# Kernel tuning notes

Hardware: AMD Instinct MI355X
Metric: run time of the kernel (lower is better)

## Reference

```python
import jax, jax.numpy as jnp
import numpy as np

N_NODES = 100000
N_EDGES = 1000000
D = 64
N_LAYERS = 3
LN_EPS = 1e-5


def setup_inputs() -> dict:
    key = jax.random.key(0)
    ks = jax.random.split(key, 12)
    s = 1.0 / np.sqrt(D)
    return {
        "feats": jax.random.normal(ks[0], (N_NODES, D), jnp.float32),
        "src": jax.random.randint(ks[1], (N_EDGES,), 0, N_NODES, jnp.int32),
        "dst": jax.random.randint(ks[2], (N_EDGES,), 0, N_NODES, jnp.int32),
        # GraphConv weights/biases (stacked over layers; in==hid==out==D)
        "conv_W": jax.random.normal(ks[3], (N_LAYERS, D, D), jnp.float32) * s,
        "conv_b": jnp.zeros((N_LAYERS, D), jnp.float32),
        # residual Linear per layer
        "res_W": jax.random.normal(ks[4], (N_LAYERS, D, D), jnp.float32) * s,
        "res_b": jnp.zeros((N_LAYERS, D), jnp.float32),
        # LayerNorm affine per layer
        "ln_g": jnp.ones((N_LAYERS, D), jnp.float32),
        "ln_b": jnp.zeros((N_LAYERS, D), jnp.float32),
        # final linear_prediction
        "pred_W": jax.random.normal(ks[5], (D, D), jnp.float32) * s,
        "pred_b": jnp.zeros((D,), jnp.float32),
    }


def _layer_norm(h, g, b):
    mu = jnp.mean(h, axis=-1, keepdims=True)
    var = jnp.mean(jnp.square(h - mu), axis=-1, keepdims=True)
    return (h - mu) * jax.lax.rsqrt(var + LN_EPS) * g + b


def reference(feats, src, dst, conv_W, conv_b, res_W, res_b, ln_g, ln_b, pred_W, pred_b):
    n = feats.shape[0]
    ones = jnp.ones(src.shape[0], feats.dtype)
    # DGL GraphConv norm='both', degrees clamped to >= 1
    out_deg = jnp.clip(jax.ops.segment_sum(ones, src, num_segments=n), 1.0, None)
    in_deg = jnp.clip(jax.ops.segment_sum(ones, dst, num_segments=n), 1.0, None)
    out_norm = jax.lax.rsqrt(out_deg)[:, None]  # [N,1]
    in_norm = jax.lax.rsqrt(in_deg)[:, None]

    h = feats
    h_final = jnp.zeros_like(feats)
    for i in range(N_LAYERS):
        # GraphConv: scale src, sum-aggregate over edges, scale dst, linear
        msg = (h * out_norm)[src]                                   # [E, D]
        agg = jax.ops.segment_sum(msg, dst, num_segments=n) * in_norm
        conv = agg @ conv_W[i] + conv_b[i]
        # residual linear + LayerNorm + relu (dropout p=0) + JK accumulate
        h = conv + h @ res_W[i] + res_b[i]
        h = jax.nn.relu(_layer_norm(h, ln_g[i], ln_b[i]))
        h_final = h_final + h
    return h_final @ pred_W + pred_b
```

## Files before the change

kernel.cpp:

```cpp
#include <hip/hip_runtime.h>
#include <hip/hip_bf16.h>

#define DD 64
#define NBLK 128
#define MAXBUK 1024
#define BSHIFT 7
#define NB3 64

typedef __attribute__((ext_vector_type(8))) short short8v;
typedef __attribute__((ext_vector_type(4))) float f32x4;

__device__ __forceinline__ unsigned pk_bf16(float a, float b) {
    __hip_bfloat162 h = __float22bfloat162_rn(make_float2(a, b));
    unsigned u; __builtin_memcpy(&u, &h, 4); return u;
}
__device__ __forceinline__ short f2bf_s(float f) {
    union { float f; unsigned u; } x; x.f = f;
    unsigned r = x.u + 0x7fff + ((x.u >> 16) & 1);
    return (short)(r >> 16);
}
__device__ __forceinline__ float bf_lo(unsigned u) { return __int_as_float(u << 16); }
__device__ __forceinline__ float bf_hi(unsigned u) { return __int_as_float(u & 0xffff0000u); }
__device__ __forceinline__ short8v u4_to_s8(uint4 u) {
    union { uint4 u; short8v s; } x; x.u = u; return x.s;
}


__global__ __launch_bounds__(256) void part_count(
        const int* __restrict__ src, const int* __restrict__ dst,
        int* __restrict__ cnt, int E, int nbuk, int ce) {
    __shared__ int hd[MAXBUK], hs[MAXBUK];
    for (int i = threadIdx.x; i < MAXBUK; i += 256) { hd[i] = 0; hs[i] = 0; }
    __syncthreads();
    int e0 = blockIdx.x * ce;
    int e1 = min(e0 + ce, E);
    for (int e = e0 + (int)threadIdx.x; e < e1; e += 256) {
        atomicAdd(&hd[dst[e] >> BSHIFT], 1);
        atomicAdd(&hs[src[e] >> BSHIFT], 1);
    }
    __syncthreads();
    int L2 = nbuk * NBLK;
    for (int b = threadIdx.x; b < nbuk; b += 256) {
        cnt[b * NBLK + blockIdx.x]      = hd[b];
        cnt[L2 + b * NBLK + blockIdx.x] = hs[b];
    }
}

__global__ void scan1p(int* __restrict__ a, int* __restrict__ bsums, int L) {
    __shared__ int tmp[256];
    int gid = blockIdx.x * 256 + threadIdx.x;
    int v = (gid < L) ? a[gid] : 0;
    tmp[threadIdx.x] = v;
    __syncthreads();
    for (int off = 1; off < 256; off <<= 1) {
        int t = (threadIdx.x >= off) ? tmp[threadIdx.x - off] : 0;
        __syncthreads();
        tmp[threadIdx.x] += t;
        __syncthreads();
    }
    if (gid < L) a[gid] = tmp[threadIdx.x] - v;
    if (threadIdx.x == 255) bsums[blockIdx.x] = tmp[255];
}
__global__ void scan2p(int* __restrict__ bsums, int nb) {
    __shared__ int tmp[1024];
    int v = (threadIdx.x < (unsigned)nb) ? bsums[threadIdx.x] : 0;
    tmp[threadIdx.x] = v;
    __syncthreads();
    for (int off = 1; off < 1024; off <<= 1) {
        int t = (threadIdx.x >= off) ? tmp[threadIdx.x - off] : 0;
        __syncthreads();
        tmp[threadIdx.x] += t;
        __syncthreads();
    }
    if (threadIdx.x < (unsigned)nb) bsums[threadIdx.x] = tmp[threadIdx.x] - v;
}
__global__ void scan3p(int* __restrict__ a, const int* __restrict__ bsums, int L) {
    int gid = blockIdx.x * 256 + threadIdx.x;
    if (gid < L) a[gid] += bsums[blockIdx.x];
}

__global__ __launch_bounds__(256) void part_scatter(
        const int* __restrict__ src, const int* __restrict__ dst,
        const int* __restrict__ ofs,
        unsigned int* __restrict__ partD, unsigned char* __restrict__ partS,
        int E, int nbuk, int ce) {
    __shared__ int cd[MAXBUK], cs[MAXBUK];
    int L2 = nbuk * NBLK;
    for (int b = threadIdx.x; b < nbuk; b += 256) {
        cd[b] = ofs[b * NBLK + blockIdx.x];
        cs[b] = ofs[L2 + b * NBLK + blockIdx.x] - E;
    }
    __syncthreads();
    int e0 = blockIdx.x * ce;
    int e1 = min(e0 + ce, E);
    for (int e = e0 + (int)threadIdx.x; e < e1; e += 256) {
        int s = src[e], d = dst[e];
        int pd = atomicAdd(&cd[d >> BSHIFT], 1);
        partD[pd] = ((unsigned)(d & 127) << 17) | (unsigned)s;
        int ps = atomicAdd(&cs[s >> BSHIFT], 1);
        partS[ps] = (unsigned char)(s & 127);
    }
}

__global__ __launch_bounds__(256) void bucket_hist(
        const unsigned int* __restrict__ partD, const int* __restrict__ ofs,
        int* __restrict__ deg, int E, int nbuk, int n) {
    __shared__ int h[128];
    int b = blockIdx.x, tid = threadIdx.x;
    int e0 = ofs[b * NBLK];
    int e1 = (b + 1 < nbuk) ? ofs[(b + 1) * NBLK] : E;
    if (tid < 128) h[tid] = 0;
    __syncthreads();
    for (int e = e0 + tid; e < e1; e += 256)
        atomicAdd(&h[partD[e] >> 17], 1);
    __syncthreads();
    if (tid < 128) {
        int v = (b << BSHIFT) + tid;
        if (v < n) deg[v] = h[tid];
    }
}

__global__ __launch_bounds__(256) void bucket_deg(
        const unsigned char* __restrict__ partS, const int* __restrict__ ofs,
        int* __restrict__ outdeg, int E, int nbuk, int n) {
    __shared__ int h[128];
    int b = blockIdx.x, tid = threadIdx.x;
    int L2 = nbuk * NBLK;
    int f0 = ofs[L2 + b * NBLK] - E;
    int f1 = (b + 1 < nbuk) ? ofs[L2 + (b + 1) * NBLK] - E : E;
    if (tid < 128) h[tid] = 0;
    __syncthreads();
    for (int e = f0 + tid; e < f1; e += 256)
        atomicAdd(&h[(int)partS[e]], 1);
    __syncthreads();
    if (tid < 128) {
        int v = (b << BSHIFT) + tid;
        if (v < n) outdeg[v] = h[tid];
    }
}

__global__ __launch_bounds__(256) void dhist(const int* __restrict__ deg,
                                             int* __restrict__ cnt2, int N, int chunk) {
    __shared__ int h2[256];
    h2[threadIdx.x] = 0;
    __syncthreads();
    int b = blockIdx.x;
    int v0 = b * chunk, v1 = min(v0 + chunk, N);
    for (int v = v0 + (int)threadIdx.x; v < v1; v += 256)
        atomicAdd(&h2[min(deg[v], 255)], 1);
    __syncthreads();
    cnt2[threadIdx.x * NB3 + b] = h2[threadIdx.x];
}
__global__ __launch_bounds__(256) void dscatter(const int* __restrict__ deg,
                                                const int* __restrict__ cnt2,
                                                int* __restrict__ perm, int N, int chunk) {
    __shared__ int cu2[256];
    int b = blockIdx.x;
    cu2[threadIdx.x] = cnt2[threadIdx.x * NB3 + b];
    __syncthreads();
    int v0 = b * chunk, v1 = min(v0 + chunk, N);
    for (int v = v0 + (int)threadIdx.x; v < v1; v += 256) {
        int pos = atomicAdd(&cu2[min(deg[v], 255)], 1);
        perm[pos] = v;
    }
}
__global__ void invperm(const int* __restrict__ perm, int* __restrict__ inv, int N) {
    int i = blockIdx.x * 256 + threadIdx.x;
    if (i < N) inv[perm[i]] = i;
}
__global__ void sortgath(const int* __restrict__ perm, const int* __restrict__ deg,
                         const int* __restrict__ outdeg,
                         int* __restrict__ rowptr2, float* __restrict__ inn2,
                         float* __restrict__ rs2, float* __restrict__ outn2,
                         int N, int E) {
    int i = blockIdx.x * 256 + threadIdx.x;
    if (i < N) {
        int p = perm[i];
        int d = deg[p];
        int od = outdeg[p];
        rowptr2[i] = d;
        inn2[i] = rsqrtf((float)max(d, 1));
        float odc = (float)max(od, 1);
        outn2[i] = rsqrtf(odc);
        rs2[i]   = sqrtf(odc);
        if (i == 0) rowptr2[N] = E;
    }
}

__global__ __launch_bounds__(256) void bucket_scatter(
        const unsigned int* __restrict__ partD, const int* __restrict__ ofs,
        const int* __restrict__ rowptr2, const int* __restrict__ inv,
        int* __restrict__ esrc2, int E, int nbuk, int n) {
    __shared__ int cu[128];
    int b = blockIdx.x, tid = threadIdx.x;
    int e0 = ofs[b * NBLK];
    int e1 = (b + 1 < nbuk) ? ofs[(b + 1) * NBLK] : E;
    if (tid < 128) {
        int v = (b << BSHIFT) + tid;
        cu[tid] = (v < n) ? rowptr2[inv[v]] : 0;
    }
    __syncthreads();
    for (int e = e0 + tid; e < e1; e += 256) {
        unsigned u = partD[e];
        int p = atomicAdd(&cu[u >> 17], 1);
        esrc2[p] = inv[u & 0x1FFFFu];
    }
}

__global__ void scale_perm(const float* __restrict__ feats, const float* __restrict__ outn2,
                           const int* __restrict__ perm,
                           unsigned short* __restrict__ hs, int n) {
    int idx = blockIdx.x * blockDim.x + threadIdx.x;
    if (idx < n * 8) {
        int v = idx >> 3, c = idx & 7;
        int p = perm[v];
        float s = outn2[v];
        const float4* fp = (const float4*)(feats + (size_t)p * DD) + c * 2;
        float4 f0 = fp[0], f1 = fp[1];
        uint4 o;
        o.x = pk_bf16(f0.x * s, f0.y * s); o.y = pk_bf16(f0.z * s, f0.w * s);
        o.z = pk_bf16(f1.x * s, f1.y * s); o.w = pk_bf16(f1.z * s, f1.w * s);
        ((uint4*)hs)[idx] = o;
    }
}

__global__ __launch_bounds__(256) void gcn_kernel(
    const int* __restrict__ rowptr, const int* __restrict__ esrc,
    const int* __restrict__ perm,
    const float* __restrict__ inn, const float* __restrict__ rs,
    const float* __restrict__ outn,
    const unsigned short* __restrict__ hs_in,
    const float* __restrict__ Wc, const float* __restrict__ bc,
    const float* __restrict__ Wr, const float* __restrict__ br,
    const float* __restrict__ Wp, const float* __restrict__ pb,
    const float* __restrict__ g, const float* __restrict__ bb,
    unsigned short* __restrict__ hs_out, float* __restrict__ h_final,
    float* __restrict__ pred_out,
    int first, int last, int n)
{
    __shared__ __align__(16) short sWf[24 * 64 * 8];
    __shared__ __align__(16) short sXa[4][16 * 72];
    __shared__ float sEps[4 * 64];

    int lane = threadIdx.x & 63;
    int wave = threadIdx.x >> 6;
    int q   = lane & 15;
    int gg  = lane >> 4;
    int q8  = lane & 7;
    int o8  = lane >> 3;

    for (int idx = threadIdx.x; idx < 64; idx += blockDim.x) {
        sEps[idx]       = bc[idx] + br[idx];
        sEps[64 + idx]  = g[idx];
        sEps[128 + idx] = bb[idx];
        sEps[192 + idx] = pb[idx];
    }
    for (int f = wave * 6; f < wave * 6 + 6; ++f) {
        int mat = f >> 3, ft = (f >> 1) & 3, kc = f & 1;
        const float* Ws = (mat == 0) ? Wc : (mat == 1) ? Wr : Wp;
        int feat = ft * 16 + q;
        int k0 = kc * 32 + gg * 8;
        short8v fr;
        #pragma unroll
        for (int j = 0; j < 8; ++j) fr[j] = f2bf_s(Ws[(k0 + j) * DD + feat]);
        *(short8v*)&sWf[(f * 64 + lane) * 8] = fr;
    }
    __syncthreads();

    short* xrow_w = &sXa[wave][0];
    const short8v* wf = (const short8v*)sWf;
    int wgid = blockIdx.x * 4 + wave;
    int nwav = gridDim.x * 4;
    int ngrp = (n + 15) >> 4;

    for (int grp = wgid; grp < ngrp; grp += nwav) {
        int vbase = grp << 4;
        int vo = vbase + q;
        int vsel = min(vo, n - 1);

        const uint4* hrow = (const uint4*)(hs_in + (size_t)vsel * DD);
        uint4 bh0u = hrow[gg];
        uint4 bh1u = hrow[4 + gg];
        float rsv  = rs[vsel];
        float innv = inn[vsel];

        int rp = rowptr[min(vbase + min(lane, 16), n)];
        int stA = __shfl(rp, o8);     int dgA = __shfl(rp, o8 + 1) - stA;
        int stB = __shfl(rp, o8 + 8); int dgB = __shfl(rp, o8 + 9) - stB;

        #pragma unroll
        for (int hh = 0; hh < 2; ++hh) {
            int st = hh ? stB : stA;
            int dg = hh ? dgB : dgA;
            int mdg = dg;
            mdg = max(mdg, __shfl_xor(mdg, 8));
            mdg = max(mdg, __shfl_xor(mdg, 16));
            mdg = max(mdg, __shfl_xor(mdg, 32));

            float a[8];
            #pragma unroll
            for (int c = 0; c < 8; ++c) a[c] = 0.0f;

            int id0 = (0 < dg) ? esrc[st + 0] : 0;  float m0 = (0 < dg) ? 1.f : 0.f;
            int id1 = (1 < dg) ? esrc[st + 1] : 0;  float m1 = (1 < dg) ? 1.f : 0.f;
            int id2 = (2 < dg) ? esrc[st + 2] : 0;  float m2 = (2 < dg) ? 1.f : 0.f;
            int id3 = (3 < dg) ? esrc[st + 3] : 0;  float m3 = (3 < dg) ? 1.f : 0.f;

            for (int t = 0; t < mdg; t += 4) {
                uint4 r0 = *(const uint4*)(hs_in + (size_t)id0 * DD + q8 * 8);
                uint4 r1 = *(const uint4*)(hs_in + (size_t)id1 * DD + q8 * 8);
                uint4 r2 = *(const uint4*)(hs_in + (size_t)id2 * DD + q8 * 8);
                uint4 r3 = *(const uint4*)(hs_in + (size_t)id3 * DD + q8 * 8);
                float c0 = m0, c1 = m1, c2 = m2, c3 = m3;
                int t4 = t + 4;
                id0 = (t4 + 0 < dg) ? esrc[st + t4 + 0] : 0;  m0 = (t4 + 0 < dg) ? 1.f : 0.f;
                id1 = (t4 + 1 < dg) ? esrc[st + t4 + 1] : 0;  m1 = (t4 + 1 < dg) ? 1.f : 0.f;
                id2 = (t4 + 2 < dg) ? esrc[st + t4 + 2] : 0;  m2 = (t4 + 2 < dg) ? 1.f : 0.f;
                id3 = (t4 + 3 < dg) ? esrc[st + t4 + 3] : 0;  m3 = (t4 + 3 < dg) ? 1.f : 0.f;
                a[0] = fmaf(bf_lo(r0.x), c0, a[0]); a[1] = fmaf(bf_hi(r0.x), c0, a[1]);
                a[2] = fmaf(bf_lo(r0.y), c0, a[2]); a[3] = fmaf(bf_hi(r0.y), c0, a[3]);
                a[4] = fmaf(bf_lo(r0.z), c0, a[4]); a[5] = fmaf(bf_hi(r0.z), c0, a[5]);
                a[6] = fmaf(bf_lo(r0.w), c0, a[6]); a[7] = fmaf(bf_hi(r0.w), c0, a[7]);
                a[0] = fmaf(bf_lo(r1.x), c1, a[0]); a[1] = fmaf(bf_hi(r1.x), c1, a[1]);
                a[2] = fmaf(bf_lo(r1.y), c1, a[2]); a[3] = fmaf(bf_hi(r1.y), c1, a[3]);
                a[4] = fmaf(bf_lo(r1.z), c1, a[4]); a[5] = fmaf(bf_hi(r1.z), c1, a[5]);
                a[6] = fmaf(bf_lo(r1.w), c1, a[6]); a[7] = fmaf(bf_hi(r1.w), c1, a[7]);
                a[0] = fmaf(bf_lo(r2.x), c2, a[0]); a[1] = fmaf(bf_hi(r2.x), c2, a[1]);
                a[2] = fmaf(bf_lo(r2.y), c2, a[2]); a[3] = fmaf(bf_hi(r2.y), c2, a[3]);
                a[4] = fmaf(bf_lo(r2.z), c2, a[4]); a[5] = fmaf(bf_hi(r2.z), c2, a[5]);
                a[6] = fmaf(bf_lo(r2.w), c2, a[6]); a[7] = fmaf(bf_hi(r2.w), c2, a[7]);
                a[0] = fmaf(bf_lo(r3.x), c3, a[0]); a[1] = fmaf(bf_hi(r3.x), c3, a[1]);
                a[2] = fmaf(bf_lo(r3.y), c3, a[2]); a[3] = fmaf(bf_hi(r3.y), c3, a[3]);
                a[4] = fmaf(bf_lo(r3.z), c3, a[4]); a[5] = fmaf(bf_hi(r3.z), c3, a[5]);
                a[6] = fmaf(bf_lo(r3.w), c3, a[6]); a[7] = fmaf(bf_hi(r3.w), c3, a[7]);
            }

            uint4 w4;
            w4.x = pk_bf16(a[0], a[1]); w4.y = pk_bf16(a[2], a[3]);
            w4.z = pk_bf16(a[4], a[5]); w4.w = pk_bf16(a[6], a[7]);
            *(uint4*)&xrow_w[(hh * 8 + o8) * 72 + q8 * 8] = w4;
        }

        const short* xr = &xrow_w[q * 72];
        short8v ba0 = *(const short8v*)&xr[gg * 8];
        short8v ba1 = *(const short8v*)&xr[32 + gg * 8];
        short8v sh0 = u4_to_s8(bh0u);
        short8v sh1 = u4_to_s8(bh1u);

        f32x4 accC[4], accR[4];
        #pragma unroll
        for (int ft = 0; ft < 4; ++ft) {
            f32x4 c = {0.f, 0.f, 0.f, 0.f};
            c = __builtin_amdgcn_mfma_f32_16x16x32_bf16(wf[(ft * 2 + 0) * 64 + lane], ba0, c, 0, 0, 0);
            c = __builtin_amdgcn_mfma_f32_16x16x32_bf16(wf[(ft * 2 + 1) * 64 + lane], ba1, c, 0, 0, 0);
            accC[ft] = c;
            f32x4 r = {0.f, 0.f, 0.f, 0.f};
            r = __builtin_amdgcn_mfma_f32_16x16x32_bf16(wf[(8 + ft * 2 + 0) * 64 + lane], sh0, r, 0, 0, 0);
            r = __builtin_amdgcn_mfma_f32_16x16x32_bf16(wf[(8 + ft * 2 + 1) * 64 + lane], sh1, r, 0, 0, 0);
            accR[ft] = r;
        }

        f32x4 ac[4];
        #pragma unroll
        for (int ft = 0; ft < 4; ++ft) {
            float4 b4 = *(const float4*)&sEps[ft * 16 + gg * 4];
            ac[ft][0] = fmaf(innv, accC[ft][0], fmaf(rsv, accR[ft][0], b4.x));
            ac[ft][1] = fmaf(innv, accC[ft][1], fmaf(rsv, accR[ft][1], b4.y));
            ac[ft][2] = fmaf(innv, accC[ft][2], fmaf(rsv, accR[ft][2], b4.z));
            ac[ft][3] = fmaf(innv, accC[ft][3], fmaf(rsv, accR[ft][3], b4.w));
        }
        float s = 0.f;
        #pragma unroll
        for (int ft = 0; ft < 4; ++ft) s += ac[ft][0] + ac[ft][1] + ac[ft][2] + ac[ft][3];
        s += __shfl_xor(s, 16); s += __shfl_xor(s, 32);
        float mu = s * (1.0f / 64.0f);
        float vsum = 0.f;
        #pragma unroll
        for (int ft = 0; ft < 4; ++ft) {
            #pragma unroll
            for (int r = 0; r < 4; ++r) { float d = ac[ft][r] - mu; vsum += d * d; }
        }
        vsum += __shfl_xor(vsum, 16); vsum += __shfl_xor(vsum, 32);
        float rinv = rsqrtf(vsum * (1.0f / 64.0f) + 1e-5f);

        float4 yv[4];
        #pragma unroll
        for (int ft = 0; ft < 4; ++ft) {
            float4 g4 = *(const float4*)&sEps[64 + ft * 16 + gg * 4];
            float4 c4 = *(const float4*)&sEps[128 + ft * 16 + gg * 4];
            yv[ft].x = fmaxf((ac[ft][0] - mu) * rinv * g4.x + c4.x, 0.f);
            yv[ft].y = fmaxf((ac[ft][1] - mu) * rinv * g4.y + c4.y, 0.f);
            yv[ft].z = fmaxf((ac[ft][2] - mu) * rinv * g4.z + c4.z, 0.f);
            yv[ft].w = fmaxf((ac[ft][3] - mu) * rinv * g4.w + c4.w, 0.f);
        }

        if (!last) {
            if (vo < n) {
                float on = outn[vo];
                #pragma unroll
                for (int ft = 0; ft < 4; ++ft) {
                    size_t off = (size_t)vo * DD + ft * 16 + gg * 4;
                    uint2 p;
                    p.x = pk_bf16(yv[ft].x * on, yv[ft].y * on);
                    p.y = pk_bf16(yv[ft].z * on, yv[ft].w * on);
                    *(uint2*)&hs_out[off] = p;
                    if (first) {
                        *(float4*)&h_final[off] = yv[ft];
                    } else {
                        float4 hf = *(const float4*)&h_final[off];
                        hf.x += yv[ft].x; hf.y += yv[ft].y;
                        hf.z += yv[ft].z; hf.w += yv[ft].w;
                        *(float4*)&h_final[off] = hf;
                    }
                }
            }
        } else {
            int pvo = perm[vsel];
            #pragma unroll
            for (int ft = 0; ft < 4; ++ft) {
                float4 hf = make_float4(0.f, 0.f, 0.f, 0.f);
                if (vo < n) {
                    float4 old = *(const float4*)&h_final[(size_t)vo * DD + ft * 16 + gg * 4];
                    hf.x = old.x + yv[ft].x; hf.y = old.y + yv[ft].y;
                    hf.z = old.z + yv[ft].z; hf.w = old.w + yv[ft].w;
                }
                uint2 p;
                p.x = pk_bf16(hf.x, hf.y);
                p.y = pk_bf16(hf.z, hf.w);
                *(uint2*)&xrow_w[q * 72 + ft * 16 + gg * 4] = p;
            }
            short8v bp0 = *(const short8v*)&xr[gg * 8];
            short8v bp1 = *(const short8v*)&xr[32 + gg * 8];
            #pragma unroll
            for (int ft = 0; ft < 4; ++ft) {
                f32x4 p = {0.f, 0.f, 0.f, 0.f};
                p = __builtin_amdgcn_mfma_f32_16x16x32_bf16(wf[(16 + ft * 2 + 0) * 64 + lane], bp0, p, 0, 0, 0);
                p = __builtin_amdgcn_mfma_f32_16x16x32_bf16(wf[(16 + ft * 2 + 1) * 64 + lane], bp1, p, 0, 0, 0);
                if (vo < n) {
                    float4 b4 = *(const float4*)&sEps[192 + ft * 16 + gg * 4];
                    float4 o = make_float4(p[0] + b4.x, p[1] + b4.y, p[2] + b4.z, p[3] + b4.w);
                    *(float4*)&pred_out[(size_t)pvo * DD + ft * 16 + gg * 4] = o;
                }
            }
        }
    }
}

extern "C" void kernel_launch(void* const* d_in, const int* in_sizes, int n_in,
                              void* d_out, int out_size, void* d_ws, size_t ws_size,
                              hipStream_t stream) {
    const float* feats  = (const float*)d_in[0];
    const int*   src    = (const int*)d_in[1];
    const int*   dst    = (const int*)d_in[2];
    const float* conv_W = (const float*)d_in[3];
    const float* conv_b = (const float*)d_in[4];
    const float* res_W  = (const float*)d_in[5];
    const float* res_b  = (const float*)d_in[6];
    const float* ln_g   = (const float*)d_in[7];
    const float* ln_b   = (const float*)d_in[8];
    const float* pred_W = (const float*)d_in[9];
    const float* pred_b = (const float*)d_in[10];

    int N = in_sizes[0] / DD;
    int E = in_sizes[1];

    int nbuk = (N + (1 << BSHIFT) - 1) >> BSHIFT;
    int ce   = (E + NBLK - 1) / NBLK;
    int L    = nbuk * NBLK * 2;
    int nb   = (L + 255) / 256;
    int chunk3 = (N + NB3 - 1) / NB3;
    int L3   = 256 * NB3;
    int nb3  = (L3 + 255) / 256;
    int nbN  = (N + 255) / 256;

    int*   rowptr2 = (int*)d_ws;
    int*   cnt    = rowptr2 + (N + 1);
    int*   bsums  = cnt + MAXBUK * NBLK * 2;
    int*   esrc2  = bsums + 1024;
    float* outn2  = (float*)(esrc2 + E);
    float* inn2   = outn2 + N;
    float* rs2    = inn2 + N;
    int*   deg    = (int*)(rs2 + N);
    int*   outdeg = deg + N;
    int*   perm   = outdeg + N;
    int*   inv    = perm + N;
    int*   cnt2   = inv + N;
    float* base   = (float*)(((uintptr_t)(cnt2 + 16384) + 15) & ~(uintptr_t)15);
    unsigned short* hsA = (unsigned short*)base;
    unsigned short* hsB = (unsigned short*)(base + (size_t)N * 32);
    float* hfin  = base + (size_t)N * 64;
    unsigned int*  partD = (unsigned int*)hfin;
    unsigned char* partS = (unsigned char*)(partD + E);

    part_count   <<<NBLK, 256, 0, stream>>>(src, dst, cnt, E, nbuk, ce);
    scan1p       <<<nb, 256, 0, stream>>>(cnt, bsums, L);
    scan2p       <<<1, 1024, 0, stream>>>(bsums, nb);
    scan3p       <<<nb, 256, 0, stream>>>(cnt, bsums, L);
    part_scatter <<<NBLK, 256, 0, stream>>>(src, dst, cnt, partD, partS, E, nbuk, ce);
    bucket_hist  <<<nbuk, 256, 0, stream>>>(partD, cnt, deg, E, nbuk, N);
    bucket_deg   <<<nbuk, 256, 0, stream>>>(partS, cnt, outdeg, E, nbuk, N);
    dhist        <<<NB3, 256, 0, stream>>>(deg, cnt2, N, chunk3);
    scan1p       <<<nb3, 256, 0, stream>>>(cnt2, bsums, L3);
    scan2p       <<<1, 1024, 0, stream>>>(bsums, nb3);
    scan3p       <<<nb3, 256, 0, stream>>>(cnt2, bsums, L3);
    dscatter     <<<NB3, 256, 0, stream>>>(deg, cnt2, perm, N, chunk3);
    invperm      <<<nbN, 256, 0, stream>>>(perm, inv, N);
    sortgath     <<<nbN, 256, 0, stream>>>(perm, deg, outdeg, rowptr2, inn2, rs2, outn2, N, E);
    scan1p       <<<nbN, 256, 0, stream>>>(rowptr2, bsums, N);
    scan2p       <<<1, 1024, 0, stream>>>(bsums, nbN);
    scan3p       <<<nbN, 256, 0, stream>>>(rowptr2, bsums, N);
    bucket_scatter<<<nbuk, 256, 0, stream>>>(partD, cnt, rowptr2, inv, esrc2, E, nbuk, N);
    scale_perm   <<<(N * 8 + 255) / 256, 256, 0, stream>>>(feats, outn2, perm, hsA, N);

    const unsigned short* ins[3]  = {hsA, hsB, hsA};
    unsigned short*       outs[3] = {hsB, hsA, hsB};
    for (int l = 0; l < 3; ++l) {
        gcn_kernel<<<1024, 256, 0, stream>>>(
            rowptr2, esrc2, perm, inn2, rs2, outn2, ins[l],
            conv_W + (size_t)l * DD * DD, conv_b + (size_t)l * DD,
            res_W  + (size_t)l * DD * DD, res_b  + (size_t)l * DD,
            pred_W, pred_b,
            ln_g   + (size_t)l * DD,      ln_b   + (size_t)l * DD,
            outs[l], hfin, (float*)d_out,
            (l == 0) ? 1 : 0, (l == 2) ? 1 : 0, N);
    }
}
```

Baseline: 326.1 us.

## Fuse preprocessing kernels, fold scan carry into consumers, sort edges per row

Merges in/out-degree histograms with the degree-bucket histogram, and fuses the degree scatter with the inverse permutation and norm gathering. Two scan-add passes are dropped by having consumers add block sums on the fly. This cuts the number of preprocessing launches and intermediate passes. It also adds a per-row quadratic sort of source indices, meant to give the gather better locality, and reverses group iteration order in the GCN kernel, at the cost of an extra kernel and O(d^2) work on high-degree rows.

New measurement: 364.1 us. 1.12x slower.

```diff
diff --git a/kernel.cpp b/kernel.cpp
--- a/kernel.cpp
+++ b/kernel.cpp
@@ -5,7 +5,6 @@
 #define NBLK 128
 #define MAXBUK 1024
 #define BSHIFT 7
-#define NB3 64
 
 typedef __attribute__((ext_vector_type(8))) short short8v;
 typedef __attribute__((ext_vector_type(4))) float f32x4;
@@ -23,6 +22,10 @@
 __device__ __forceinline__ float bf_hi(unsigned u) { return __int_as_float(u & 0xffff0000u); }
 __device__ __forceinline__ short8v u4_to_s8(uint4 u) {
     union { uint4 u; short8v s; } x; x.u = u; return x.s;
+}
+__device__ __forceinline__ int ofs_at(const int* __restrict__ c,
+                                      const int* __restrict__ bs, int i) {
+    return c[i] + bs[i >> 8];
 }
 
 
@@ -81,14 +84,14 @@
 
 __global__ __launch_bounds__(256) void part_scatter(
         const int* __restrict__ src, const int* __restrict__ dst,
-        const int* __restrict__ ofs,
+        const int* __restrict__ cnt, const int* __restrict__ bsA,
         unsigned int* __restrict__ partD, unsigned char* __restrict__ partS,
         int E, int nbuk, int ce) {
     __shared__ int cd[MAXBUK], cs[MAXBUK];
     int L2 = nbuk * NBLK;
     for (int b = threadIdx.x; b < nbuk; b += 256) {
-        cd[b] = ofs[b * NBLK + blockIdx.x];
-        cs[b] = ofs[L2 + b * NBLK + blockIdx.x] - E;
+        cd[b] = ofs_at(cnt, bsA, b * NBLK + blockIdx.x);
+        cs[b] = ofs_at(cnt, bsA, L2 + b * NBLK + blockIdx.x) - E;
     }
     __syncthreads();
     int e0 = blockIdx.x * ce;
@@ -102,99 +105,75 @@
     }
 }
 
-__global__ __launch_bounds__(256) void bucket_hist(
-        const unsigned int* __restrict__ partD, const int* __restrict__ ofs,
-        int* __restrict__ deg, int E, int nbuk, int n) {
-    __shared__ int h[128];
+__global__ __launch_bounds__(256) void bucket_histdeg(
+        const unsigned int* __restrict__ partD, const unsigned char* __restrict__ partS,
+        const int* __restrict__ cnt, const int* __restrict__ bsA,
+        int* __restrict__ deg, int* __restrict__ outdeg, int* __restrict__ cnt2,
+        int E, int nbuk, int n) {
+    __shared__ int hi[128], ho[128], h2[256];
     int b = blockIdx.x, tid = threadIdx.x;
-    int e0 = ofs[b * NBLK];
-    int e1 = (b + 1 < nbuk) ? ofs[(b + 1) * NBLK] : E;
-    if (tid < 128) h[tid] = 0;
-    __syncthreads();
+    if (tid < 128) { hi[tid] = 0; ho[tid] = 0; }
+    h2[tid] = 0;
+    __syncthreads();
+    int e0 = ofs_at(cnt, bsA, b * NBLK);
+    int e1 = (b + 1 < nbuk) ? ofs_at(cnt, bsA, (b + 1) * NBLK) : E;
     for (int e = e0 + tid; e < e1; e += 256)
-        atomicAdd(&h[partD[e] >> 17], 1);
+        atomicAdd(&hi[partD[e] >> 17], 1);
+    int L2 = nbuk * NBLK;
+    int f0 = ofs_at(cnt, bsA, L2 + b * NBLK) - E;
+    int f1 = (b + 1 < nbuk) ? ofs_at(cnt, bsA, L2 + (b + 1) * NBLK) - E : E;
+    for (int e = f0 + tid; e < f1; e += 256)
+        atomicAdd(&ho[(int)partS[e]], 1);
     __syncthreads();
     if (tid < 128) {
         int v = (b << BSHIFT) + tid;
-        if (v < n) deg[v] = h[tid];
-    }
-}
-
-__global__ __launch_bounds__(256) void bucket_deg(
-        const unsigned char* __restrict__ partS, const int* __restrict__ ofs,
-        int* __restrict__ outdeg, int E, int nbuk, int n) {
-    __shared__ int h[128];
+        if (v < n) {
+            deg[v] = hi[tid];
+            outdeg[v] = ho[tid];
+            atomicAdd(&h2[min(hi[tid], 255)], 1);
+        }
+    }
+    __syncthreads();
+    cnt2[tid * nbuk + b] = h2[tid];
+}
+
+__global__ __launch_bounds__(256) void dscatter_fused(
+        const int* __restrict__ deg, const int* __restrict__ outdeg,
+        const int* __restrict__ cnt2, const int* __restrict__ bsB,
+        int* __restrict__ perm, int* __restrict__ inv,
+        int* __restrict__ rowptr2, float* __restrict__ inn2,
+        float* __restrict__ outn2, float* __restrict__ rs2,
+        int nbuk, int n, int E) {
+    __shared__ int cu2[256];
     int b = blockIdx.x, tid = threadIdx.x;
-    int L2 = nbuk * NBLK;
-    int f0 = ofs[L2 + b * NBLK] - E;
-    int f1 = (b + 1 < nbuk) ? ofs[L2 + (b + 1) * NBLK] - E : E;
-    if (tid < 128) h[tid] = 0;
-    __syncthreads();
-    for (int e = f0 + tid; e < f1; e += 256)
-        atomicAdd(&h[(int)partS[e]], 1);
+    cu2[tid] = ofs_at(cnt2, bsB, tid * nbuk + b);
     __syncthreads();
     if (tid < 128) {
         int v = (b << BSHIFT) + tid;
-        if (v < n) outdeg[v] = h[tid];
-    }
-}
-
-__global__ __launch_bounds__(256) void dhist(const int* __restrict__ deg,
-                                             int* __restrict__ cnt2, int N, int chunk) {
-    __shared__ int h2[256];
-    h2[threadIdx.x] = 0;
-    __syncthreads();
-    int b = blockIdx.x;
-    int v0 = b * chunk, v1 = min(v0 + chunk, N);
-    for (int v = v0 + (int)threadIdx.x; v < v1; v += 256)
-        atomicAdd(&h2[min(deg[v], 255)], 1);
-    __syncthreads();
-    cnt2[threadIdx.x * NB3 + b] = h2[threadIdx.x];
-}
-__global__ __launch_bounds__(256) void dscatter(const int* __restrict__ deg,
-                                                const int* __restrict__ cnt2,
-                                                int* __restrict__ perm, int N, int chunk) {
-    __shared__ int cu2[256];
-    int b = blockIdx.x;
-    cu2[threadIdx.x] = cnt2[threadIdx.x * NB3 + b];
-    __syncthreads();
-    int v0 = b * chunk, v1 = min(v0 + chunk, N);
-    for (int v = v0 + (int)threadIdx.x; v < v1; v += 256) {
-        int pos = atomicAdd(&cu2[min(deg[v], 255)], 1);
-        perm[pos] = v;
-    }
-}
-__global__ void invperm(const int* __restrict__ perm, int* __restrict__ inv, int N) {
-    int i = blockIdx.x * 256 + threadIdx.x;
-    if (i < N) inv[perm[i]] = i;
-}
-__global__ void sortgath(const int* __restrict__ perm, const int* __restrict__ deg,
-                         const int* __restrict__ outdeg,
-                         int* __restrict__ rowptr2, float* __restrict__ inn2,
-                         float* __restrict__ rs2, float* __restrict__ outn2,
-                         int N, int E) {
-    int i = blockIdx.x * 256 + threadIdx.x;
-    if (i < N) {
-        int p = perm[i];
-        int d = deg[p];
-        int od = outdeg[p];
-        rowptr2[i] = d;
-        inn2[i] = rsqrtf((float)max(d, 1));
-        float odc = (float)max(od, 1);
-        outn2[i] = rsqrtf(odc);
-        rs2[i]   = sqrtf(odc);
-        if (i == 0) rowptr2[N] = E;
-    }
+        if (v < n) {
+            int d = deg[v];
+            int pos = atomicAdd(&cu2[min(d, 255)], 1);
+            perm[pos] = v;
+            inv[v] = pos;
+            rowptr2[pos] = d;
+            inn2[pos] = rsqrtf((float)max(d, 1));
+            float oc = (float)max(outdeg[v], 1);
+            outn2[pos] = rsqrtf(oc);
+            rs2[pos]   = sqrtf(oc);
+        }
+    }
+    if (b == 0 && tid == 0) rowptr2[n] = E;
 }
 
 __global__ __launch_bounds__(256) void bucket_scatter(
-        const unsigned int* __restrict__ partD, const int* __restrict__ ofs,
+        const unsigned int* __restrict__ partD,
+        const int* __restrict__ cnt, const int* __restrict__ bsA,
         const int* __restrict__ rowptr2, const int* __restrict__ inv,
-        int* __restrict__ esrc2, int E, int nbuk, int n) {
+        int* __restrict__ esrcT, int E, int nbuk, int n) {
     __shared__ int cu[128];
     int b = blockIdx.x, tid = threadIdx.x;
-    int e0 = ofs[b * NBLK];
-    int e1 = (b + 1 < nbuk) ? ofs[(b + 1) * NBLK] : E;
+    int e0 = ofs_at(cnt, bsA, b * NBLK);
+    int e1 = (b + 1 < nbuk) ? ofs_at(cnt, bsA, (b + 1) * NBLK) : E;
     if (tid < 128) {
         int v = (b << BSHIFT) + tid;
         cu[tid] = (v < n) ? rowptr2[inv[v]] : 0;
@@ -203,7 +182,24 @@
     for (int e = e0 + tid; e < e1; e += 256) {
         unsigned u = partD[e];
         int p = atomicAdd(&cu[u >> 17], 1);
-        esrc2[p] = inv[u & 0x1FFFFu];
+        esrcT[p] = inv[u & 0x1FFFFu];
+    }
+}
+
+__global__ void edge_sort(const int* __restrict__ rowptr2,
+                          const int* __restrict__ esrcT,
+                          int* __restrict__ esrc2, int n) {
+    int v = blockIdx.x * 256 + threadIdx.x;
+    if (v >= n) return;
+    int b0 = rowptr2[v], d = rowptr2[v + 1] - b0;
+    for (int i = 0; i < d; ++i) {
+        int ki = esrcT[b0 + i];
+        int pos = 0;
+        for (int j = 0; j < d; ++j) {
+            int kj = esrcT[b0 + j];
+            pos += (kj < ki) | ((kj == ki) & (j < i));
+        }
+        esrc2[b0 + pos] = ki;
     }
 }
 
@@ -273,7 +269,8 @@
     int nwav = gridDim.x * 4;
     int ngrp = (n + 15) >> 4;
 
-    for (int grp = wgid; grp < ngrp; grp += nwav) {
+    for (int g0 = wgid; g0 < ngrp; g0 += nwav) {
+        int grp = ngrp - 1 - g0;
         int vbase = grp << 4;
         int vo = vbase + q;
         int vsel = min(vo, n - 1);
@@ -468,49 +465,47 @@
     int ce   = (E + NBLK - 1) / NBLK;
     int L    = nbuk * NBLK * 2;
     int nb   = (L + 255) / 256;
-    int chunk3 = (N + NB3 - 1) / NB3;
-    int L3   = 256 * NB3;
+    int L3   = 256 * nbuk;
     int nb3  = (L3 + 255) / 256;
     int nbN  = (N + 255) / 256;
 
     int*   rowptr2 = (int*)d_ws;
     int*   cnt    = rowptr2 + (N + 1);
-    int*   bsums  = cnt + MAXBUK * NBLK * 2;
-    int*   esrc2  = bsums + 1024;
+    int*   bsA    = cnt + MAXBUK * NBLK * 2;
+    int*   bsB    = bsA + 1024;
+    int*   bsC    = bsB + 1024;
+    int*   esrc2  = bsC + 1024;
     float* outn2  = (float*)(esrc2 + E);
     float* inn2   = outn2 + N;
     float* rs2    = inn2 + N;
-    int*   deg    = (int*)(rs2 + N);
-    int*   outdeg = deg + N;
-    int*   perm   = outdeg + N;
-    int*   inv    = perm + N;
-    int*   cnt2   = inv + N;
-    float* base   = (float*)(((uintptr_t)(cnt2 + 16384) + 15) & ~(uintptr_t)15);
+    int*   perm   = (int*)(rs2 + N);
+    float* base   = (float*)(((uintptr_t)(perm + N) + 15) & ~(uintptr_t)15);
     unsigned short* hsA = (unsigned short*)base;
     unsigned short* hsB = (unsigned short*)(base + (size_t)N * 32);
     float* hfin  = base + (size_t)N * 64;
     unsigned int*  partD = (unsigned int*)hfin;
     unsigned char* partS = (unsigned char*)(partD + E);
-
-    part_count   <<<NBLK, 256, 0, stream>>>(src, dst, cnt, E, nbuk, ce);
-    scan1p       <<<nb, 256, 0, stream>>>(cnt, bsums, L);
-    scan2p       <<<1, 1024, 0, stream>>>(bsums, nb);
-    scan3p       <<<nb, 256, 0, stream>>>(cnt, bsums, L);
-    part_scatter <<<NBLK, 256, 0, stream>>>(src, dst, cnt, partD, partS, E, nbuk, ce);
-    bucket_hist  <<<nbuk, 256, 0, stream>>>(partD, cnt, deg, E, nbuk, N);
-    bucket_deg   <<<nbuk, 256, 0, stream>>>(partS, cnt, outdeg, E, nbuk, N);
-    dhist        <<<NB3, 256, 0, stream>>>(deg, cnt2, N, chunk3);
-    scan1p       <<<nb3, 256, 0, stream>>>(cnt2, bsums, L3);
-    scan2p       <<<1, 1024, 0, stream>>>(bsums, nb3);
-    scan3p       <<<nb3, 256, 0, stream>>>(cnt2, bsums, L3);
-    dscatter     <<<NB3, 256, 0, stream>>>(deg, cnt2, perm, N, chunk3);
-    invperm      <<<nbN, 256, 0, stream>>>(perm, inv, N);
-    sortgath     <<<nbN, 256, 0, stream>>>(perm, deg, outdeg, rowptr2, inn2, rs2, outn2, N, E);
-    scan1p       <<<nbN, 256, 0, stream>>>(rowptr2, bsums, N);
-    scan2p       <<<1, 1024, 0, stream>>>(bsums, nbN);
-    scan3p       <<<nbN, 256, 0, stream>>>(rowptr2, bsums, N);
-    bucket_scatter<<<nbuk, 256, 0, stream>>>(partD, cnt, rowptr2, inv, esrc2, E, nbuk, N);
-    scale_perm   <<<(N * 8 + 255) / 256, 256, 0, stream>>>(feats, outn2, perm, hsA, N);
+    int* cnt2   = (int*)hsB;
+    int* deg    = cnt2 + 256 * MAXBUK;
+    int* outdeg = deg + N;
+    int* inv    = outdeg + N;
+    int* esrcT  = (int*)hsA;
+
+    part_count    <<<NBLK, 256, 0, stream>>>(src, dst, cnt, E, nbuk, ce);
+    scan1p        <<<nb, 256, 0, stream>>>(cnt, bsA, L);
+    scan2p        <<<1, 1024, 0, stream>>>(bsA, nb);
+    part_scatter  <<<NBLK, 256, 0, stream>>>(src, dst, cnt, bsA, partD, partS, E, nbuk, ce);
+    bucket_histdeg<<<nbuk, 256, 0, stream>>>(partD, partS, cnt, bsA, deg, outdeg, cnt2, E, nbuk, N);
+    scan1p        <<<nb3, 256, 0, stream>>>(cnt2, bsB, L3);
+    scan2p        <<<1, 1024, 0, stream>>>(bsB, nb3);
+    dscatter_fused<<<nbuk, 256, 0, stream>>>(deg, outdeg, cnt2, bsB, perm, inv,
+                                             rowptr2, inn2, outn2, rs2, nbuk, N, E);
+    scan1p        <<<nbN, 256, 0, stream>>>(rowptr2, bsC, N);
+    scan2p        <<<1, 1024, 0, stream>>>(bsC, nbN);
+    scan3p        <<<nbN, 256, 0, stream>>>(rowptr2, bsC, N);
+    bucket_scatter<<<nbuk, 256, 0, stream>>>(partD, cnt, bsA, rowptr2, inv, esrcT, E, nbuk, N);
+    edge_sort     <<<nbN, 256, 0, stream>>>(rowptr2, esrcT, esrc2, N);
+    scale_perm    <<<(N * 8 + 255) / 256, 256, 0, stream>>>(feats, outn2, perm, hsA, N);
 
     const unsigned short* ins[3]  = {hsA, hsB, hsA};
     unsigned short*       outs[3] = {hsB, hsA, hsB};
```
